# Kernel tuning notes

Measured on AMD Instinct MI355X. Metric: run time of the kernel, lower is better.

## Reference

```python
import jax, jax.numpy as jnp
import numpy as np

IOU_THR = 0.5      # global_nms default
SCORE_THR = 0.5    # global_nms default
SCORE_BONUS = 0.05 # _match_queries_to_prompt_boxes combined score bonus


def _box_iou_matrix(a, b):
    # a: [P,4], b: [Q,4] in xyxy
    lt = jnp.maximum(a[:, None, :2], b[None, :, :2])
    rb = jnp.minimum(a[:, None, 2:], b[None, :, 2:])
    wh = jnp.clip(rb - lt, 0.0)
    inter = wh[..., 0] * wh[..., 1]
    area_a = jnp.clip(a[:, 2] - a[:, 0], 0.0) * jnp.clip(a[:, 3] - a[:, 1], 0.0)
    area_b = jnp.clip(b[:, 2] - b[:, 0], 0.0) * jnp.clip(b[:, 3] - b[:, 1], 0.0)
    union = area_a[:, None] + area_b[None, :] - inter
    return jnp.where(union > 0.0, inter / union, 0.0)


def _rand_boxes(key, n, size):
    pts = jax.random.uniform(key, (n, 2, 2)) * size
    lt = jnp.min(pts, axis=1)
    rb = jnp.max(pts, axis=1)
    return jnp.concatenate([lt, rb], axis=-1)


def setup_inputs() -> dict:
    key = jax.random.key(0)
    k1, k2, k3, k4 = jax.random.split(key, 4)
    N, H, W, P = 96, 512, 512, 8
    mask_logits = jax.random.normal(k1, (N, H, W), dtype=jnp.float32)
    scores = jax.random.uniform(k2, (N,), dtype=jnp.float32)
    prompt_boxes = _rand_boxes(k3, P, float(W)).astype(jnp.float32)
    query_boxes = _rand_boxes(k4, N, float(W)).astype(jnp.float32)
    return {"mask_logits": mask_logits, "scores": scores,
            "prompt_boxes": prompt_boxes, "query_boxes": query_boxes}


def reference(mask_logits, scores, prompt_boxes, query_boxes):
    N = mask_logits.shape[0]
    # ---- pairwise mask IoU (batched, replaces per-pair mask_iou + .item syncs) ----
    m = (mask_logits > 0.0).astype(mask_logits.dtype).reshape(N, -1)  # [N,HW]
    inter = m @ m.T                                                    # [N,N]
    area = m.sum(-1)
    union = area[:, None] + area[None, :] - inter
    iou = jnp.where(union > 0.0, inter / union, 0.0)

    # ---- greedy mask NMS (global_nms) ----
    eligible = scores >= SCORE_THR
    eligible = jnp.where(jnp.any(eligible), eligible, jnp.ones_like(eligible))
    order = jnp.argsort(-scores)            # descending score, like pairs.sort
    iou_s = iou[order][:, order]
    elig_s = eligible[order]

    def nms_step(kept, i):
        sup = jnp.any(kept & (iou_s[i] > IOU_THR))
        k_i = elig_s[i] & (~sup)
        return kept.at[i].set(k_i), None

    kept_s, _ = jax.lax.scan(nms_step, jnp.zeros((N,), bool), jnp.arange(N))
    keep = jnp.zeros((N,), bool).at[order].set(kept_s)
    nms_scores = scores * keep.astype(scores.dtype)   # [N]

    # ---- greedy box-to-query bipartite matching ----
    bi = _box_iou_matrix(prompt_boxes, query_boxes)   # [P,Q]
    combined = bi + SCORE_BONUS * scores[None, :]
    P, Q = combined.shape
    flat_order = jnp.argsort(-combined.reshape(-1))   # candidates, best first
    ps = flat_order // Q
    qs = flat_order % Q

    def match_step(state, pq):
        assigned, used, assign = state
        p, q = pq
        take = (~assigned[p]) & (~used[q])
        assigned = assigned.at[p].set(assigned[p] | take)
        used = used.at[q].set(used[q] | take)
        assign = assign.at[p].set(jnp.where(take, q, assign[p]))
        return (assigned, used, assign), None

    init = (jnp.zeros((P,), bool), jnp.zeros((Q,), bool),
            jnp.full((P,), -1, dtype=jnp.int32))
    (assigned, used, assign), _ = jax.lax.scan(match_step, init,
                                               (ps.astype(jnp.int32), qs.astype(jnp.int32)))

    # fallback: unmatched prompts take highest-score unused query
    def fb_step(state, p):
        used, assign = state
        need = assign[p] < 0
        q = jnp.argmax(jnp.where(used, -jnp.inf, scores)).astype(jnp.int32)
        assign = assign.at[p].set(jnp.where(need, q, assign[p]))
        used = used.at[q].set(used[q] | need)
        return (used, assign), None

    (used, assign), _ = jax.lax.scan(fb_step, (used, assign), jnp.arange(P))
    matched_combined = combined[jnp.arange(P), assign]  # [P]

    return jnp.concatenate([nms_scores, matched_combined])
```

## Files before the change

kernel.cpp:

```cpp
#include <hip/hip_runtime.h>
#include <cstdint>
#include <cstddef>

#define N_MASKS 96
#define HW (512 * 512)
#define WORDS_PER_ROW (HW / 64)
#define VECS_PER_ROW (WORDS_PER_ROW / 2)
#define TOTAL_WORDS (N_MASKS * WORDS_PER_ROW)
#define P_BOXES 8
#define SCORE_THR 0.5f
#define SCORE_BONUS 0.05f
#define TILE 4
#define NT (N_MASKS / TILE)
#define ACTIVE_TILES (NT * (NT + 1) / 2)

__global__ __launch_bounds__(256) void pack_kernel(
    const float4* __restrict__ logits,
    unsigned long long* __restrict__ bits,
    int* counter) {
  if (blockIdx.x == 0 && threadIdx.x == 0) *counter = 0;
  int wave = (blockIdx.x * blockDim.x + threadIdx.x) >> 6;
  int lane = threadIdx.x & 63;
  size_t g0 = (size_t)wave * 4;
  float4 v0 = logits[(g0 + 0) * 64 + lane];
  float4 v1 = logits[(g0 + 1) * 64 + lane];
  float4 v2 = logits[(g0 + 2) * 64 + lane];
  float4 v3 = logits[(g0 + 3) * 64 + lane];
  unsigned long long m[16];
  m[0]  = __ballot(v0.x > 0.0f); m[1]  = __ballot(v0.y > 0.0f);
  m[2]  = __ballot(v0.z > 0.0f); m[3]  = __ballot(v0.w > 0.0f);
  m[4]  = __ballot(v1.x > 0.0f); m[5]  = __ballot(v1.y > 0.0f);
  m[6]  = __ballot(v1.z > 0.0f); m[7]  = __ballot(v1.w > 0.0f);
  m[8]  = __ballot(v2.x > 0.0f); m[9]  = __ballot(v2.y > 0.0f);
  m[10] = __ballot(v2.z > 0.0f); m[11] = __ballot(v2.w > 0.0f);
  m[12] = __ballot(v3.x > 0.0f); m[13] = __ballot(v3.y > 0.0f);
  m[14] = __ballot(v3.z > 0.0f); m[15] = __ballot(v3.w > 0.0f);
  if (lane == 0) {
    unsigned long long* dst = bits + g0 * 4;
#pragma unroll
    for (int k = 0; k < 16; ++k) dst[k] = m[k];
  }
}

__global__ __launch_bounds__(256) void inter_finalize_kernel(
    const unsigned long long* __restrict__ bits,
    int* inter, int* counter,
    const float* __restrict__ scores,
    const float* __restrict__ pboxes,
    const float* __restrict__ qboxes,
    float* __restrict__ out) {
  __shared__ int red[4][TILE * TILE];
  __shared__ bool s_last;
  __shared__ int s_int[N_MASKS * N_MASKS];
  __shared__ float s_scores[N_MASKS];
  __shared__ int s_order[N_MASKS];
  __shared__ float s_comb[P_BOXES * N_MASKS];
  __shared__ float s_pb[P_BOXES * 4];
  __shared__ float s_qb[N_MASKS * 4];

  int t = threadIdx.x;

  int b = blockIdx.x, ty = 0;
  while (b >= NT - ty) { b -= NT - ty; ++ty; }
  int tx = ty + b;
  int bi = ty * TILE, bj = tx * TILE;

  const ulonglong2* base = (const ulonglong2*)bits;
  int acc[TILE * TILE];
#pragma unroll
  for (int k = 0; k < TILE * TILE; ++k) acc[k] = 0;
#pragma unroll
  for (int w = 0; w < VECS_PER_ROW / 256; ++w) {
    int idx = w * 256 + t;
    ulonglong2 a[TILE], bb[TILE];
#pragma unroll
    for (int r = 0; r < TILE; ++r)
      a[r] = base[(size_t)(bi + r) * VECS_PER_ROW + idx];
#pragma unroll
    for (int c = 0; c < TILE; ++c)
      bb[c] = base[(size_t)(bj + c) * VECS_PER_ROW + idx];
#pragma unroll
    for (int r = 0; r < TILE; ++r)
#pragma unroll
      for (int c = 0; c < TILE; ++c)
        acc[r * TILE + c] += __popcll(a[r].x & bb[c].x) + __popcll(a[r].y & bb[c].y);
  }
#pragma unroll
  for (int k = 0; k < TILE * TILE; ++k)
    for (int off = 32; off >= 1; off >>= 1) acc[k] += __shfl_xor(acc[k], off);
  int wv = t >> 6;
  if ((t & 63) == 0) {
#pragma unroll
    for (int k = 0; k < TILE * TILE; ++k) red[wv][k] = acc[k];
  }
  __syncthreads();
  if (t < TILE * TILE) {
    int tot = red[0][t] + red[1][t] + red[2][t] + red[3][t];
    int i = bi + (t >> 2), j = bj + (t & 3);
    if (j >= i) {
      __hip_atomic_store(&inter[i * N_MASKS + j], tot, __ATOMIC_RELAXED, __HIP_MEMORY_SCOPE_AGENT);
      __hip_atomic_store(&inter[j * N_MASKS + i], tot, __ATOMIC_RELAXED, __HIP_MEMORY_SCOPE_AGENT);
    }
  }
  __syncthreads();
  if (t == 0) {
    int ticket = __hip_atomic_fetch_add(counter, 1, __ATOMIC_ACQ_REL, __HIP_MEMORY_SCOPE_AGENT);
    s_last = (ticket == ACTIVE_TILES - 1);
  }
  __syncthreads();
  if (!s_last) return;

  if (t < N_MASKS) s_scores[t] = scores[t];
  for (int k = t; k < P_BOXES * 4; k += 256) s_pb[k] = pboxes[k];
  for (int k = t; k < N_MASKS * 4; k += 256) s_qb[k] = qboxes[k];
  for (int e = t; e < N_MASKS * N_MASKS; e += 256)
    s_int[e] = __hip_atomic_load(&inter[e], __ATOMIC_RELAXED, __HIP_MEMORY_SCOPE_AGENT);
  __syncthreads();

  if (t < N_MASKS) {
    float sc = s_scores[t];
    int r = 0;
    for (int m = 0; m < N_MASKS; ++m) {
      float sm = s_scores[m];
      if (sm > sc || (sm == sc && m < t)) ++r;
    }
    s_order[r] = t;
  }
  for (int f = t; f < P_BOXES * N_MASKS; f += 256) {
    int p = f / N_MASKS, q = f % N_MASKS;
    float ax0 = s_pb[p * 4 + 0], ay0 = s_pb[p * 4 + 1];
    float ax1 = s_pb[p * 4 + 2], ay1 = s_pb[p * 4 + 3];
    float bx0 = s_qb[q * 4 + 0], by0 = s_qb[q * 4 + 1];
    float bx1 = s_qb[q * 4 + 2], by1 = s_qb[q * 4 + 3];
    float ltx = fmaxf(ax0, bx0), lty = fmaxf(ay0, by0);
    float rbx = fminf(ax1, bx1), rby = fminf(ay1, by1);
    float w = fmaxf(rbx - ltx, 0.0f), h = fmaxf(rby - lty, 0.0f);
    float in_ = w * h;
    float aa = fmaxf(ax1 - ax0, 0.0f) * fmaxf(ay1 - ay0, 0.0f);
    float ab = fmaxf(bx1 - bx0, 0.0f) * fmaxf(by1 - by0, 0.0f);
    float un = aa + ab - in_;
    float iou = (un > 0.0f) ? in_ / un : 0.0f;
    s_comb[f] = iou + SCORE_BONUS * s_scores[q];
  }
  __syncthreads();

  if (t < 64) {
    int lane = t;
    int oc1 = s_order[lane];
    int oc2 = (lane < 32) ? s_order[lane + 64] : 0;
    int a1 = s_int[oc1 * N_MASKS + oc1];
    int a2 = s_int[oc2 * N_MASKS + oc2];
    unsigned long long c1_lo = 0, c1_hi = 0, c2_lo = 0, c2_hi = 0;
    for (int i = 0; i < N_MASKS; ++i) {
      int oi = s_order[i];
      int ai = s_int[oi * N_MASKS + oi];
      bool t1 = 3 * s_int[oi * N_MASKS + oc1] > ai + a1;
      bool t2 = (lane < 32) && (3 * s_int[oi * N_MASKS + oc2] > ai + a2);
      unsigned long long bit = 1ull << (i & 63);
      if (i < 64) { if (t1) c1_lo |= bit; if (t2) c2_lo |= bit; }
      else        { if (t1) c1_hi |= bit; if (t2) c2_hi |= bit; }
    }
    unsigned long long el_lo = __ballot(s_scores[oc1] >= SCORE_THR);
    unsigned long long el_hi = __ballot((lane < 32) && (s_scores[oc2] >= SCORE_THR));
    if ((el_lo | el_hi) == 0ull) { el_lo = ~0ull; el_hi = ~0ull; }

    bool k1 = false, k2 = false;
    for (int i = 0; i < N_MASKS; ++i) {
      bool c;
      bool el;
      if (i < 64) {
        unsigned long long bit = 1ull << i;
        c = (k1 && (c1_lo & bit)) || (k2 && (c2_lo & bit));
        el = (el_lo >> i) & 1ull;
      } else {
        unsigned long long bit = 1ull << (i - 64);
        c = (k1 && (c1_hi & bit)) || (k2 && (c2_hi & bit));
        el = (el_hi >> (i - 64)) & 1ull;
      }
      bool sup = __any(c);
      bool ki = el && !sup;
      if (lane == i) k1 = ki;
      if (lane + 64 == i) k2 = ki;
    }
    out[oc1] = k1 ? s_scores[oc1] : 0.0f;
    if (lane < 32) out[oc2] = k2 ? s_scores[oc2] : 0.0f;
  } else if (t < 128) {
    int lane = t & 63;
    unsigned assigned_p = 0;
    unsigned long long used_lo = 0, used_hi = 0;
    int assign_q[P_BOXES];
#pragma unroll
    for (int p = 0; p < P_BOXES; ++p) assign_q[p] = -1;

    for (int it = 0; it < P_BOXES; ++it) {
      float bv = -1.0f;
      int bf = 1 << 30;
#pragma unroll
      for (int k = 0; k < (P_BOXES * N_MASKS) / 64; ++k) {
        int f = lane + 64 * k;
        int p = f / N_MASKS, q = f % N_MASKS;
        bool pv = !((assigned_p >> p) & 1u);
        bool qv = (q < 64) ? !((used_lo >> q) & 1ull) : !((used_hi >> (q - 64)) & 1ull);
        if (pv && qv) {
          float v = s_comb[f];
          if (v > bv || (v == bv && f < bf)) { bv = v; bf = f; }
        }
      }
      for (int off = 32; off >= 1; off >>= 1) {
        float ov = __shfl_xor(bv, off);
        int of = __shfl_xor(bf, off);
        if (ov > bv || (ov == bv && of < bf)) { bv = ov; bf = of; }
      }
      if (bf < (1 << 30)) {
        int p = bf / N_MASKS, q = bf % N_MASKS;
        assigned_p |= 1u << p;
        if (q < 64) used_lo |= 1ull << q;
        else used_hi |= 1ull << (q - 64);
        assign_q[p] = q;
      }
    }
#pragma unroll
    for (int p = 0; p < P_BOXES; ++p) {
      if (assign_q[p] < 0) {
        float best = -1e30f;
        int bq = 0;
        for (int q = 0; q < N_MASKS; ++q) {
          bool used = (q < 64) ? ((used_lo >> q) & 1ull) : ((used_hi >> (q - 64)) & 1ull);
          float v = used ? -1e30f : s_scores[q];
          if (v > best) { best = v; bq = q; }
        }
        assign_q[p] = bq;
        if (bq < 64) used_lo |= 1ull << bq;
        else used_hi |= 1ull << (bq - 64);
      }
    }
#pragma unroll
    for (int p = 0; p < P_BOXES; ++p) {
      if (lane == p) out[N_MASKS + p] = s_comb[p * N_MASKS + assign_q[p]];
    }
  }
}

extern "C" void kernel_launch(void* const* d_in, const int* in_sizes, int n_in,
                              void* d_out, int out_size, void* d_ws, size_t ws_size,
                              hipStream_t stream) {
  const float* mask_logits = (const float*)d_in[0];
  const float* scores = (const float*)d_in[1];
  const float* pboxes = (const float*)d_in[2];
  const float* qboxes = (const float*)d_in[3];
  float* out = (float*)d_out;

  unsigned long long* bits = (unsigned long long*)d_ws;
  int* inter = (int*)((char*)d_ws + (size_t)TOTAL_WORDS * sizeof(unsigned long long));
  int* counter = inter + N_MASKS * N_MASKS;

  int total_waves = (TOTAL_WORDS / 4) / 4;
  int pack_blocks = (total_waves * 64) / 256;
  pack_kernel<<<pack_blocks, 256, 0, stream>>>((const float4*)mask_logits, bits, counter);

  inter_finalize_kernel<<<ACTIVE_TILES, 256, 0, stream>>>(
      bits, inter, counter, scores, pboxes, qboxes, out);
}
```

Baseline: 70.25 us.

## Split fused last-block finalize into separate intersection and finalize kernels

Replaces the atomic-counter last-block pattern with three kernel launches: pack, a 2D-grid intersection kernel that early-exits lower-triangle tiles, and a single 128-thread finalize kernel. This removes the atomic ticket, the atomic loads and stores, and the large shared-memory footprint that every intersection block carried only so one block could do the finalize. In exchange it adds one extra kernel launch and a round of grid blocks that exit immediately.

```diff
diff --git a/kernel.cpp b/kernel.cpp
--- a/kernel.cpp
+++ b/kernel.cpp
@@ -11,14 +11,10 @@
 #define SCORE_THR 0.5f
 #define SCORE_BONUS 0.05f
 #define TILE 4
-#define NT (N_MASKS / TILE)
-#define ACTIVE_TILES (NT * (NT + 1) / 2)
 
 __global__ __launch_bounds__(256) void pack_kernel(
     const float4* __restrict__ logits,
-    unsigned long long* __restrict__ bits,
-    int* counter) {
-  if (blockIdx.x == 0 && threadIdx.x == 0) *counter = 0;
+    unsigned long long* __restrict__ bits) {
   int wave = (blockIdx.x * blockDim.x + threadIdx.x) >> 6;
   int lane = threadIdx.x & 63;
   size_t g0 = (size_t)wave * 4;
@@ -42,79 +38,71 @@
   }
 }
 
-__global__ __launch_bounds__(256) void inter_finalize_kernel(
+__global__ __launch_bounds__(256) void inter_kernel(
     const unsigned long long* __restrict__ bits,
-    int* inter, int* counter,
+    int* __restrict__ inter) {
+  int bi = blockIdx.y * TILE, bj = blockIdx.x * TILE;
+  if (bj + TILE - 1 < bi) return;
+  int t = threadIdx.x;
+  const ulonglong2* base = (const ulonglong2*)bits;
+  int acc[TILE * TILE];
+#pragma unroll
+  for (int k = 0; k < TILE * TILE; ++k) acc[k] = 0;
+
+#pragma unroll
+  for (int w = 0; w < VECS_PER_ROW / 256; ++w) {
+    int idx = w * 256 + t;
+    ulonglong2 a[TILE], b[TILE];
+#pragma unroll
+    for (int r = 0; r < TILE; ++r)
+      a[r] = base[(size_t)(bi + r) * VECS_PER_ROW + idx];
+#pragma unroll
+    for (int c = 0; c < TILE; ++c)
+      b[c] = base[(size_t)(bj + c) * VECS_PER_ROW + idx];
+#pragma unroll
+    for (int r = 0; r < TILE; ++r)
+#pragma unroll
+      for (int c = 0; c < TILE; ++c)
+        acc[r * TILE + c] += __popcll(a[r].x & b[c].x) + __popcll(a[r].y & b[c].y);
+  }
+#pragma unroll
+  for (int k = 0; k < TILE * TILE; ++k)
+    for (int off = 32; off >= 1; off >>= 1) acc[k] += __shfl_xor(acc[k], off);
+  __shared__ int red[4][TILE * TILE];
+  int wv = t >> 6;
+  if ((t & 63) == 0) {
+#pragma unroll
+    for (int k = 0; k < TILE * TILE; ++k) red[wv][k] = acc[k];
+  }
+  __syncthreads();
+  if (t < TILE * TILE) {
+    int tot = red[0][t] + red[1][t] + red[2][t] + red[3][t];
+    int i = bi + (t >> 2), j = bj + (t & 3);
+    if (j >= i) {
+      inter[i * N_MASKS + j] = tot;
+      inter[j * N_MASKS + i] = tot;
+    }
+  }
+}
+
+__global__ __launch_bounds__(128) void finalize_kernel(
+    const int* __restrict__ inter,
     const float* __restrict__ scores,
     const float* __restrict__ pboxes,
     const float* __restrict__ qboxes,
     float* __restrict__ out) {
-  __shared__ int red[4][TILE * TILE];
-  __shared__ bool s_last;
   __shared__ int s_int[N_MASKS * N_MASKS];
   __shared__ float s_scores[N_MASKS];
   __shared__ int s_order[N_MASKS];
   __shared__ float s_comb[P_BOXES * N_MASKS];
   __shared__ float s_pb[P_BOXES * 4];
   __shared__ float s_qb[N_MASKS * 4];
-
   int t = threadIdx.x;
 
-  int b = blockIdx.x, ty = 0;
-  while (b >= NT - ty) { b -= NT - ty; ++ty; }
-  int tx = ty + b;
-  int bi = ty * TILE, bj = tx * TILE;
-
-  const ulonglong2* base = (const ulonglong2*)bits;
-  int acc[TILE * TILE];
-#pragma unroll
-  for (int k = 0; k < TILE * TILE; ++k) acc[k] = 0;
-#pragma unroll
-  for (int w = 0; w < VECS_PER_ROW / 256; ++w) {
-    int idx = w * 256 + t;
-    ulonglong2 a[TILE], bb[TILE];
-#pragma unroll
-    for (int r = 0; r < TILE; ++r)
-      a[r] = base[(size_t)(bi + r) * VECS_PER_ROW + idx];
-#pragma unroll
-    for (int c = 0; c < TILE; ++c)
-      bb[c] = base[(size_t)(bj + c) * VECS_PER_ROW + idx];
-#pragma unroll
-    for (int r = 0; r < TILE; ++r)
-#pragma unroll
-      for (int c = 0; c < TILE; ++c)
-        acc[r * TILE + c] += __popcll(a[r].x & bb[c].x) + __popcll(a[r].y & bb[c].y);
-  }
-#pragma unroll
-  for (int k = 0; k < TILE * TILE; ++k)
-    for (int off = 32; off >= 1; off >>= 1) acc[k] += __shfl_xor(acc[k], off);
-  int wv = t >> 6;
-  if ((t & 63) == 0) {
-#pragma unroll
-    for (int k = 0; k < TILE * TILE; ++k) red[wv][k] = acc[k];
-  }
-  __syncthreads();
-  if (t < TILE * TILE) {
-    int tot = red[0][t] + red[1][t] + red[2][t] + red[3][t];
-    int i = bi + (t >> 2), j = bj + (t & 3);
-    if (j >= i) {
-      __hip_atomic_store(&inter[i * N_MASKS + j], tot, __ATOMIC_RELAXED, __HIP_MEMORY_SCOPE_AGENT);
-      __hip_atomic_store(&inter[j * N_MASKS + i], tot, __ATOMIC_RELAXED, __HIP_MEMORY_SCOPE_AGENT);
-    }
-  }
-  __syncthreads();
-  if (t == 0) {
-    int ticket = __hip_atomic_fetch_add(counter, 1, __ATOMIC_ACQ_REL, __HIP_MEMORY_SCOPE_AGENT);
-    s_last = (ticket == ACTIVE_TILES - 1);
-  }
-  __syncthreads();
-  if (!s_last) return;
-
   if (t < N_MASKS) s_scores[t] = scores[t];
-  for (int k = t; k < P_BOXES * 4; k += 256) s_pb[k] = pboxes[k];
-  for (int k = t; k < N_MASKS * 4; k += 256) s_qb[k] = qboxes[k];
-  for (int e = t; e < N_MASKS * N_MASKS; e += 256)
-    s_int[e] = __hip_atomic_load(&inter[e], __ATOMIC_RELAXED, __HIP_MEMORY_SCOPE_AGENT);
+  for (int k = t; k < P_BOXES * 4; k += 128) s_pb[k] = pboxes[k];
+  for (int k = t; k < N_MASKS * 4; k += 128) s_qb[k] = qboxes[k];
+  for (int e = t; e < N_MASKS * N_MASKS; e += 128) s_int[e] = inter[e];
   __syncthreads();
 
   if (t < N_MASKS) {
@@ -126,7 +114,7 @@
     }
     s_order[r] = t;
   }
-  for (int f = t; f < P_BOXES * N_MASKS; f += 256) {
+  for (int f = t; f < P_BOXES * N_MASKS; f += 128) {
     int p = f / N_MASKS, q = f % N_MASKS;
     float ax0 = s_pb[p * 4 + 0], ay0 = s_pb[p * 4 + 1];
     float ax1 = s_pb[p * 4 + 2], ay1 = s_pb[p * 4 + 3];
@@ -166,8 +154,7 @@
 
     bool k1 = false, k2 = false;
     for (int i = 0; i < N_MASKS; ++i) {
-      bool c;
-      bool el;
+      bool c, el;
       if (i < 64) {
         unsigned long long bit = 1ull << i;
         c = (k1 && (c1_lo & bit)) || (k2 && (c2_lo & bit));
@@ -184,7 +171,7 @@
     }
     out[oc1] = k1 ? s_scores[oc1] : 0.0f;
     if (lane < 32) out[oc2] = k2 ? s_scores[oc2] : 0.0f;
-  } else if (t < 128) {
+  } else {
     int lane = t & 63;
     unsigned assigned_p = 0;
     unsigned long long used_lo = 0, used_hi = 0;
@@ -252,12 +239,13 @@
 
   unsigned long long* bits = (unsigned long long*)d_ws;
   int* inter = (int*)((char*)d_ws + (size_t)TOTAL_WORDS * sizeof(unsigned long long));
-  int* counter = inter + N_MASKS * N_MASKS;
 
   int total_waves = (TOTAL_WORDS / 4) / 4;
   int pack_blocks = (total_waves * 64) / 256;
-  pack_kernel<<<pack_blocks, 256, 0, stream>>>((const float4*)mask_logits, bits, counter);
-
-  inter_finalize_kernel<<<ACTIVE_TILES, 256, 0, stream>>>(
-      bits, inter, counter, scores, pboxes, qboxes, out);
-}
+  pack_kernel<<<pack_blocks, 256, 0, stream>>>((const float4*)mask_logits, bits);
+
+  dim3 g2(N_MASKS / TILE, N_MASKS / TILE);
+  inter_kernel<<<g2, 256, 0, stream>>>(bits, inter);
+
+  finalize_kernel<<<1, 128, 0, stream>>>(inter, scores, pboxes, qboxes, out);
+}
```

Result: faster. 62.41 us (-11.2%).
